# Kernel tuning notes

Measured on AMD Instinct MI355X. Metric: run time of the kernel, lower is better.

The kernel has to match this reference:

```python
import jax, jax.numpy as jnp
import numpy as np

C = 1.0          # Poincare ball curvature
EPS = 1e-7
MAX_TANH_ARG = 1.0 - 1e-5
K = 5            # topk neighbors (hardcoded in the module)


def _norm(x):
    return jnp.clip(jnp.linalg.norm(x, axis=-1, keepdims=True), EPS)


def expmap0(u):
    # exp map at origin: tanh(sqrt(c)||u||) * u / (sqrt(c)||u||)
    sc = jnp.sqrt(C)
    n = _norm(u)
    return jnp.tanh(sc * n) * u / (sc * n)


def logmap0(x):
    # log map at origin: artanh(sqrt(c)||x||) * x / (sqrt(c)||x||)
    sc = jnp.sqrt(C)
    n = _norm(x)
    arg = jnp.clip(sc * n, EPS, MAX_TANH_ARG)
    return jnp.arctanh(arg) * x / (sc * n)


def mobius_add(x, y):
    x2 = jnp.sum(x * x, axis=-1, keepdims=True)
    y2 = jnp.sum(y * y, axis=-1, keepdims=True)
    xy = jnp.sum(x * y, axis=-1, keepdims=True)
    num = (1.0 + 2.0 * C * xy + C * y2) * x + (1.0 - C * x2) * y
    den = 1.0 + 2.0 * C * xy + (C * C) * x2 * y2
    return num / (den + EPS)


def setup_inputs() -> dict:
    key = jax.random.key(0)
    k1, k2, k3, k4 = jax.random.split(key, 4)
    B, SEQ_DIM, HYP_DIM, N = 2048, 768, 128, 100000
    z_seq = jax.random.normal(k1, (B, SEQ_DIM), dtype=jnp.float32)
    # node embeddings must lie inside the unit ball; scale keeps norms ~0.57
    node_emb = 0.05 * jax.random.normal(k2, (N, HYP_DIM), dtype=jnp.float32)
    W = 0.02 * jax.random.normal(k3, (HYP_DIM, SEQ_DIM), dtype=jnp.float32)
    b = jnp.zeros((HYP_DIM,), dtype=jnp.float32)
    return {"z_seq": z_seq, "node_emb": node_emb, "W": W, "b": b}


def reference(z_seq, node_emb, W, b):
    # linear projection (dropout is identity in eval mode)
    z_proj = z_seq @ W.T + b                     # (B, D)
    z_hyp = expmap0(z_proj)                      # (B, D) in Poincare ball
    # no-grad nearest-node lookup in tangent space
    z_tan = logmap0(z_hyp)                       # (B, D)
    n_tan = logmap0(node_emb)                    # (N, D)
    # squared euclidean distances (monotone in cdist -> same topk indices)
    d2 = (jnp.sum(z_tan * z_tan, axis=-1, keepdims=True)
          - 2.0 * (z_tan @ n_tan.T)
          + jnp.sum(n_tan * n_tan, axis=-1)[None, :])  # (B, N)
    _, idx = jax.lax.top_k(-d2, K)               # (B, K) smallest distances
    near = jnp.mean(node_emb[idx], axis=1)       # (B, D) gather-mean
    z_fused = mobius_add(z_hyp, near)
    return (z_fused, z_hyp)
```

## Files before the change

kernel.cpp:

```cpp
#include <hip/hip_runtime.h>
#include <hip/hip_bf16.h>
#include <math.h>

#define EPSF 1e-7f
#define MAXT 0.99999f

typedef __attribute__((ext_vector_type(8))) short short8v;
typedef __attribute__((ext_vector_type(4))) float f32x4;

constexpr int Bb = 2048;
constexpr int Ss = 768;
constexpr int Dd = 128;
constexpr int Nn = 100000;
constexpr int Kk = 5;
constexpr int HALF = Bb * Dd;
constexpr int NT = 128;
constexpr int TILE_BYTES = NT * Dd * 2;
constexpr int SUP_BYTES = 2 * TILE_BYTES;
constexpr float SBIAS = 16.0f;

constexpr int NCH8 = 8;
constexpr int CH8 = Nn / NCH8;
constexpr int TIL8 = 98;
constexpr int NSUP = TIL8 / 2;
constexpr int PAD8 = TIL8 * NT;
constexpr int RQ = 64;

constexpr int NCH16 = 16;
constexpr int CH16 = Nn / NCH16;
constexpr int TIL16 = (CH16 + NT - 1) / NT;
constexpr int RT = 128;

static __device__ __forceinline__ ushort f2bf(float x) {
  __hip_bfloat16 h = __float2bfloat16(x);
  return *reinterpret_cast<ushort*>(&h);
}

static __device__ __forceinline__ float med3f(float a, float b, float c) {
  float r;
  asm("v_med3_f32 %0, %1, %2, %3" : "=v"(r) : "v"(a), "v"(b), "v"(c));
  return r;
}

static __device__ __forceinline__ void ins5f(float* k, float v) {
  const float n0 = fminf(k[0], v);
  const float n1 = med3f(k[0], k[1], v);
  const float n2 = med3f(k[1], k[2], v);
  const float n3 = med3f(k[2], k[3], v);
  const float n4 = med3f(k[3], k[4], v);
  k[0] = n0; k[1] = n1; k[2] = n2; k[3] = n3; k[4] = n4;
}

#define INS5(TV, TI, V, ID) do { \
  const float _v = (V); const int _id = (ID); \
  if (_v < TV[4]) { \
    TV[4] = _v; TI[4] = _id; \
    if (TV[4] < TV[3]) { float _t=TV[3];TV[3]=TV[4];TV[4]=_t;int _u=TI[3];TI[3]=TI[4];TI[4]=_u; } \
    if (TV[3] < TV[2]) { float _t=TV[2];TV[2]=TV[3];TV[3]=_t;int _u=TI[2];TI[2]=TI[3];TI[3]=_u; } \
    if (TV[2] < TV[1]) { float _t=TV[1];TV[1]=TV[2];TV[2]=_t;int _u=TI[1];TI[1]=TI[2];TI[2]=_u; } \
    if (TV[1] < TV[0]) { float _t=TV[0];TV[0]=TV[1];TV[1]=_t;int _u=TI[0];TI[0]=TI[1];TI[1]=_u; } \
  } } while(0)

#define LXLT(V,I,V2,I2) ((V) < (V2) || ((V) == (V2) && (I) < (I2)))
#define INS5L(TV, TI, V, ID) do { \
  const float _v = (V); const int _id = (ID); \
  if (LXLT(_v,_id,TV[4],TI[4])) { \
    TV[4]=_v; TI[4]=_id; \
    if (LXLT(TV[4],TI[4],TV[3],TI[3])) { float _t=TV[3];TV[3]=TV[4];TV[4]=_t;int _u=TI[3];TI[3]=TI[4];TI[4]=_u; } \
    if (LXLT(TV[3],TI[3],TV[2],TI[2])) { float _t=TV[2];TV[2]=TV[3];TV[3]=_t;int _u=TI[2];TI[2]=TI[3];TI[3]=_u; } \
    if (LXLT(TV[2],TI[2],TV[1],TI[1])) { float _t=TV[1];TV[1]=TV[2];TV[2]=_t;int _u=TI[1];TI[1]=TI[2];TI[2]=_u; } \
    if (LXLT(TV[1],TI[1],TV[0],TI[0])) { float _t=TV[0];TV[0]=TV[1];TV[1]=_t;int _u=TI[0];TI[0]=TI[1];TI[1]=_u; } \
  } } while(0)

static __device__ __forceinline__ void proj_body(
    const float* __restrict__ zseq, const float* __restrict__ W,
    const float* __restrict__ bias, float* __restrict__ outH,
    ushort* __restrict__ ztb, int blk,
    float (*zrow)[768], float (*zp)[128], float (*php)[128], float* rno)
{
  const int tid = threadIdx.x;
  const int d = tid & 127, h = tid >> 7;
  const int r0 = blk * 8;

  {
    const float4* src = reinterpret_cast<const float4*>(zseq + (size_t)r0 * Ss);
    float4* dst = reinterpret_cast<float4*>(&zrow[0][0]);
    #pragma unroll
    for (int i = 0; i < 6; ++i) dst[i * 256 + tid] = src[i * 256 + tid];
  }
  __syncthreads();

  float acc[8];
  #pragma unroll
  for (int r = 0; r < 8; ++r) acc[r] = 0.f;
  const float4* w4 = reinterpret_cast<const float4*>(W + (size_t)d * Ss) + h * 96;
  for (int j = 0; j < 96; ++j) {
    const float4 w = w4[j];
    const int kb = h * 384 + j * 4;
    #pragma unroll
    for (int r = 0; r < 8; ++r) {
      const float4 z = *reinterpret_cast<const float4*>(&zrow[r][kb]);
      acc[r] = fmaf(z.x, w.x, acc[r]);
      acc[r] = fmaf(z.y, w.y, acc[r]);
      acc[r] = fmaf(z.z, w.z, acc[r]);
      acc[r] = fmaf(z.w, w.w, acc[r]);
    }
  }
  #pragma unroll
  for (int r = 0; r < 8; ++r) {
    if (h == 0) zp[r][d] = acc[r]; else php[r][d] = acc[r];
  }
  __syncthreads();
  if (tid < 128) {
    const float bv = bias[d];
    #pragma unroll
    for (int r = 0; r < 8; ++r) zp[r][d] = zp[r][d] + php[r][d] + bv;
  }
  __syncthreads();

  const int wv = tid >> 6, ln = tid & 63;
  if (tid < 128) {
    #pragma unroll
    for (int rr = 0; rr < 4; ++rr) {
      const int r = wv * 4 + rr;
      float v = zp[r][ln] * zp[r][ln] + zp[r][ln + 64] * zp[r][ln + 64];
      #pragma unroll
      for (int off = 32; off > 0; off >>= 1) v += __shfl_xor(v, off);
      if (ln == 0) rno[r] = v;
    }
  }
  __syncthreads();
  if (tid < 128) {
    #pragma unroll
    for (int r = 0; r < 8; ++r) {
      const float n = fmaxf(sqrtf(rno[r]), EPSF);
      const float zh = tanhf(n) * zp[r][d] / n;
      outH[(size_t)(r0 + r) * Dd + d] = zh;
      zp[r][d] = zh;
    }
  }
  __syncthreads();
  if (tid < 128) {
    #pragma unroll
    for (int rr = 0; rr < 4; ++rr) {
      const int r = wv * 4 + rr;
      float v = zp[r][ln] * zp[r][ln] + zp[r][ln + 64] * zp[r][ln + 64];
      #pragma unroll
      for (int off = 32; off > 0; off >>= 1) v += __shfl_xor(v, off);
      if (ln == 0) rno[r] = v;
    }
  }
  __syncthreads();
  if (tid < 128) {
    #pragma unroll
    for (int r = 0; r < 8; ++r) {
      const float m = fmaxf(sqrtf(rno[r]), EPSF);
      const float a = atanhf(fminf(m, MAXT));
      ztb[(size_t)(r0 + r) * Dd + d] = f2bf(a * zp[r][d] / m);
    }
  }
}

__global__ __launch_bounds__(256) void k_proj(
    const float* __restrict__ zseq, const float* __restrict__ W,
    const float* __restrict__ bias, float* __restrict__ outH,
    ushort* __restrict__ ztb)
{
  __shared__ __align__(16) float zrow[8][768];
  __shared__ float zp[8][128];
  __shared__ float php[8][128];
  __shared__ float rno[8];
  proj_body(zseq, W, bias, outH, ztb, blockIdx.x, zrow, zp, php, rno);
}

__global__ __launch_bounds__(256) void k_prep(
    const float* __restrict__ zseq, const float* __restrict__ W,
    const float* __restrict__ bias, float* __restrict__ outH,
    ushort* __restrict__ ztb, const float* __restrict__ emb,
    ushort* __restrict__ embsw, float* __restrict__ cpad)
{
  __shared__ __align__(16) float zrow[8][768];
  __shared__ float zp[8][128];
  __shared__ float php[8][128];
  __shared__ float rno[8];

  if (blockIdx.x < Bb / 8) {
    proj_body(zseq, W, bias, outH, ztb, blockIdx.x, zrow, zp, php, rno);
    return;
  }

  const int wv = threadIdx.x >> 6, ln = threadIdx.x & 63;
  const int p = (blockIdx.x - Bb / 8) * 4 + wv;
  const int chunk = p / PAD8;
  const int local = p - chunk * PAD8;
  const bool real = local < CH8;
  const int node = chunk * CH8 + local;
  float2 v = make_float2(0.f, 0.f);
  if (real) v = *reinterpret_cast<const float2*>(emb + (size_t)node * Dd + ln * 2);
  float t = v.x * v.x + v.y * v.y;
  #pragma unroll
  for (int off = 32; off > 0; off >>= 1) t += __shfl_xor(t, off);

  const float E = fmaxf(sqrtf(t), EPSF);
  const float a = atanhf(fminf(E, MAXT));
  const float s = a / E;
  const float m2s = -2.f * s;

  const int tt = local >> 7, nd = local & 127;
  ushort2 w; w.x = f2bf(m2s * v.x); w.y = f2bf(m2s * v.y);
  char* dst = reinterpret_cast<char*>(embsw)
            + ((size_t)((chunk * TIL8 + tt) * NT + nd) << 8)
            + ((ln * 4) ^ ((nd & 7) << 4));
  *reinterpret_cast<ushort2*>(dst) = w;

  if (ln == 0) cpad[p] = real ? (s * s * t + SBIAS) : 3.0e38f;
}

__global__ __launch_bounds__(1024, 4) void k_topk8(
    const ushort* __restrict__ ztb, const ushort* __restrict__ embsw,
    const float* __restrict__ cpad, float* __restrict__ candV,
    int* __restrict__ candI)
{
  __shared__ __align__(16) ushort Bsm[2][2][NT * Dd];
  __shared__ __align__(16) float cb[2][2 * NT];

  const int tid = threadIdx.x;
  const int ln = tid & 63;
  const int wv8 = (tid >> 6) & 7;
  const int qh = tid >> 9;
  const int ln15 = ln & 15;
  const int g = ln >> 4;
  const int chunk = blockIdx.x & 7;
  const int rowBase = (blockIdx.x >> 3) * RQ;
  const int qBase = rowBase + qh * 32;
  const char* embc = reinterpret_cast<const char*>(embsw)
                   + (size_t)chunk * (TIL8 * TILE_BYTES);
  const float* cch = cpad + (size_t)chunk * PAD8;

  short8v zfr[2][4];
  #pragma unroll
  for (int f = 0; f < 2; ++f)
    #pragma unroll
    for (int ks = 0; ks < 4; ++ks)
      zfr[f][ks] = *reinterpret_cast<const short8v*>(
          ztb + (size_t)(qBase + 16 * f + ln15) * Dd + 32 * ks + 8 * g);

  int rdoff[4];
  #pragma unroll
  for (int ks = 0; ks < 4; ++ks)
    rdoff[ks] = (wv8 * 16 + ln15) * 256 + ((ks * 64 + g * 16) ^ ((ln15 & 7) << 4));
  const int coff = wv8 * 64 + g * 16;
  const unsigned lanebase = (unsigned)(wv8 * 16 + 4 * g);

  float tv0[5], tv1[5];
  const float KINIT = __uint_as_float(0x7F7FFFFFu);
  #pragma unroll
  for (int q = 0; q < 5; ++q) { tv0[q] = KINIT; tv1[q] = KINIT; }

  const char* srcP = embc + tid * 16;
  const float* cbP = cch + tid;

  auto stage = [&](int buf) {
    char* lb = reinterpret_cast<char*>(&Bsm[buf][0][0]) + tid * 16;
    #pragma unroll
    for (int i = 0; i < 4; ++i) {
      __builtin_amdgcn_global_load_lds(
          (const __attribute__((address_space(1))) unsigned int*)(srcP + i * 16384),
          (__attribute__((address_space(3))) unsigned int*)(lb + i * 16384),
          16, 0, 0);
    }
    if (tid < 2 * NT) {
      __builtin_amdgcn_global_load_lds(
          (const __attribute__((address_space(1))) unsigned int*)cbP,
          (__attribute__((address_space(3))) unsigned int*)(&cb[buf][tid]),
          4, 0, 0);
    }
    srcP += SUP_BYTES;
    cbP += 2 * NT;
  };

  asm volatile("s_waitcnt vmcnt(0)" ::: "memory");
  stage(0);
  stage(1);

  for (int st = 0; st < NSUP; ++st) {
    const int buf = st & 1;
    if (st == NSUP - 1) {
      asm volatile("s_waitcnt vmcnt(0)" ::: "memory");
    } else if (tid < 2 * NT) {
      asm volatile("s_waitcnt vmcnt(5)" ::: "memory");
    } else {
      asm volatile("s_waitcnt vmcnt(4)" ::: "memory");
    }
    __builtin_amdgcn_s_barrier();

    float mm0 = KINIT, mm1 = KINIT;
    #pragma unroll
    for (int u = 0; u < 2; ++u) {
      const char* bbase = reinterpret_cast<const char*>(&Bsm[buf][u][0]);
      short8v ae[4];
      #pragma unroll
      for (int ks = 0; ks < 4; ++ks)
        ae[ks] = *reinterpret_cast<const short8v*>(bbase + rdoff[ks]);
      const f32x4 cinit = *reinterpret_cast<const f32x4*>(
          reinterpret_cast<const char*>(&cb[buf][u * NT]) + coff);

      __builtin_amdgcn_s_setprio(1);
      f32x4 a0 = __builtin_amdgcn_mfma_f32_16x16x32_bf16(ae[0], zfr[0][0], cinit, 0, 0, 0);
      f32x4 a1 = __builtin_amdgcn_mfma_f32_16x16x32_bf16(ae[0], zfr[1][0], cinit, 0, 0, 0);
      #pragma unroll
      for (int ks = 1; ks < 4; ++ks) {
        a0 = __builtin_amdgcn_mfma_f32_16x16x32_bf16(ae[ks], zfr[0][ks], a0, 0, 0, 0);
        a1 = __builtin_amdgcn_mfma_f32_16x16x32_bf16(ae[ks], zfr[1][ks], a1, 0, 0, 0);
      }
      __builtin_amdgcn_s_setprio(0);

      const unsigned ib = (unsigned)((2 * st + u) * NT) + lanebase;
      {
        const float k0 = __uint_as_float((__float_as_uint(a0[0]) & 0xFFFFC000u) | ib);
        const float k1 = __uint_as_float((__float_as_uint(a0[1]) & 0xFFFFC000u) | (ib + 1));
        const float k2 = __uint_as_float((__float_as_uint(a0[2]) & 0xFFFFC000u) | (ib + 2));
        const float k3 = __uint_as_float((__float_as_uint(a0[3]) & 0xFFFFC000u) | (ib + 3));
        mm0 = fminf(mm0, fminf(fminf(k0, k1), fminf(k2, k3)));
      }
      {
        const float k0 = __uint_as_float((__float_as_uint(a1[0]) & 0xFFFFC000u) | ib);
        const float k1 = __uint_as_float((__float_as_uint(a1[1]) & 0xFFFFC000u) | (ib + 1));
        const float k2 = __uint_as_float((__float_as_uint(a1[2]) & 0xFFFFC000u) | (ib + 2));
        const float k3 = __uint_as_float((__float_as_uint(a1[3]) & 0xFFFFC000u) | (ib + 3));
        mm1 = fminf(mm1, fminf(fminf(k0, k1), fminf(k2, k3)));
      }
    }
    ins5f(tv0, mm0);
    ins5f(tv1, mm1);

    __builtin_amdgcn_s_barrier();
    asm volatile("" ::: "memory");
    if (st + 2 < NSUP) stage(buf);
  }

  #pragma unroll
  for (int m = 16; m <= 32; m <<= 1) {
    float ov[5];
    #pragma unroll
    for (int q = 0; q < 5; ++q) ov[q] = __shfl_xor(tv0[q], m);
    #pragma unroll
    for (int q = 0; q < 5; ++q) ins5f(tv0, ov[q]);
    #pragma unroll
    for (int q = 0; q < 5; ++q) ov[q] = __shfl_xor(tv1[q], m);
    #pragma unroll
    for (int q = 0; q < 5; ++q) ins5f(tv1, ov[q]);
  }
  __syncthreads();
  float* mgk = reinterpret_cast<float*>(&Bsm[0][0][0]);
  if (ln < 16) {
    #pragma unroll
    for (int q = 0; q < 5; ++q) {
      mgk[((qh * 32 + 0 + ln) * 8 + wv8) * Kk + q] = tv0[q];
      mgk[((qh * 32 + 16 + ln) * 8 + wv8) * Kk + q] = tv1[q];
    }
  }
  __syncthreads();
  if (tid < RQ) {
    float mv[5];
    #pragma unroll
    for (int q = 0; q < 5; ++q) mv[q] = mgk[(tid * 8 + 0) * Kk + q];
    for (int w = 1; w < 8; ++w)
      #pragma unroll
      for (int q = 0; q < 5; ++q) ins5f(mv, mgk[(tid * 8 + w) * Kk + q]);
    const size_t o = ((size_t)(rowBase + tid) * NCH8 + chunk) * Kk;
    #pragma unroll
    for (int q = 0; q < 5; ++q) {
      const unsigned u = __float_as_uint(mv[q]);
      candV[o + q] = __uint_as_float(u & 0xFFFFC000u);
      candI[o + q] = chunk * CH8 + (int)(u & 0x3FFFu);
    }
  }
}

__global__ __launch_bounds__(256) void k_node(
    const float* __restrict__ emb, float* __restrict__ sArr, float* __restrict__ cArr)
{
  const int wv = threadIdx.x >> 6, ln = threadIdx.x & 63;
  const int node = blockIdx.x * 4 + wv;
  const float2 v = *reinterpret_cast<const float2*>(emb + (size_t)node * Dd + ln * 2);
  float t = v.x * v.x + v.y * v.y;
  #pragma unroll
  for (int off = 32; off > 0; off >>= 1) t += __shfl_xor(t, off);
  if (ln == 0) {
    const float E = fmaxf(sqrtf(t), EPSF);
    const float a = atanhf(fminf(E, MAXT));
    const float s = a / E;
    sArr[node] = s;
    cArr[node] = s * s * t;
  }
}

__global__ __launch_bounds__(512, 2) void k_topk16(
    const ushort* __restrict__ ztb, const float* __restrict__ emb,
    const float* __restrict__ sArr, const float* __restrict__ cArr,
    float* __restrict__ candV, int* __restrict__ candI)
{
  __shared__ __align__(16) ushort Bsm[2][NT * Dd];
  __shared__ __align__(16) float2 sclb[2][NT];
  __shared__ __align__(16) float mgv[RT][2][Kk];
  __shared__ int mgi[RT][2][Kk];

  const int tid = threadIdx.x;
  const int ln = tid & 63;
  const int wv = tid >> 6;
  const int ln15 = ln & 15;
  const int g = ln >> 4;
  const int wr = wv >> 1;
  const int wc = wv & 1;
  const int rowBase = blockIdx.x * RT;
  const int chunkStart = blockIdx.y * CH16;

  short8v afr[2][4];
  #pragma unroll
  for (int f = 0; f < 2; ++f)
    #pragma unroll
    for (int ks = 0; ks < 4; ++ks)
      afr[f][ks] = *reinterpret_cast<const short8v*>(
          ztb + (size_t)(rowBase + 32 * wr + 16 * f + ln15) * Dd + 32 * ks + 8 * g);

  int rdoff[4];
  #pragma unroll
  for (int ks = 0; ks < 4; ++ks)
    rdoff[ks] = (wc * 64 + ln15) * 256 + ((g * 16 + ks * 64) ^ ((ln15 & 7) << 4));

  f32x4 acc[2][4];
  #pragma unroll
  for (int f = 0; f < 2; ++f)
    #pragma unroll
    for (int c = 0; c < 4; ++c) acc[f][c] = (f32x4)0.f;

  float tv[8][5]; int ti[8][5];
  #pragma unroll
  for (int r = 0; r < 8; ++r)
    #pragma unroll
    for (int q = 0; q < 5; ++q) { tv[r][q] = 3.0e38f; ti[r][q] = 0x7fffffff; }

  float4 ld[8];

  auto stageLoad = [&](int t) {
    const int tStart = t * NT;
    const int left = CH16 - tStart;
    #pragma unroll
    for (int i = 0; i < 8; ++i) {
      const int flat = i * 512 + tid;
      const int nd = flat >> 5;
      float4 v = make_float4(0.f, 0.f, 0.f, 0.f);
      if (nd < left)
        v = *reinterpret_cast<const float4*>(
            emb + (size_t)(chunkStart + tStart + nd) * Dd + (flat & 31) * 4);
      ld[i] = v;
    }
  };

  auto stageWrite = [&](int t, int buf) {
    char* base = reinterpret_cast<char*>(&Bsm[buf][0]);
    #pragma unroll
    for (int i = 0; i < 8; ++i) {
      const int flat = i * 512 + tid;
      const int nd = flat >> 5;
      const int kb = (flat & 31) * 8;
      ushort4 w;
      w.x = f2bf(ld[i].x); w.y = f2bf(ld[i].y);
      w.z = f2bf(ld[i].z); w.w = f2bf(ld[i].w);
      *reinterpret_cast<ushort4*>(base + nd * 256 + (kb ^ ((nd & 7) << 4))) = w;
    }
    const int tStart = t * NT;
    const int left = CH16 - tStart;
    if (tid < NT) {
      const bool ok = tid < left;
      sclb[buf][tid] = make_float2(ok ? -2.f * sArr[chunkStart + tStart + tid] : 0.f,
                                   ok ? cArr[chunkStart + tStart + tid] : 3.0e38f);
    }
  };

  stageLoad(0);
  stageWrite(0, 0);
  __syncthreads();

  for (int t = 0; t < TIL16; ++t) {
    const int buf = t & 1;
    const bool have = (t + 1) < TIL16;
    if (have) stageLoad(t + 1);

    const char* bbase = reinterpret_cast<const char*>(&Bsm[buf][0]);
    #pragma unroll
    for (int c = 0; c < 4; ++c) {
      #pragma unroll
      for (int ks = 0; ks < 4; ++ks) {
        const short8v bfr = *reinterpret_cast<const short8v*>(bbase + c * 4096 + rdoff[ks]);
        acc[0][c] = __builtin_amdgcn_mfma_f32_16x16x32_bf16(afr[0][ks], bfr, acc[0][c], 0, 0, 0);
        acc[1][c] = __builtin_amdgcn_mfma_f32_16x16x32_bf16(afr[1][ks], bfr, acc[1][c], 0, 0, 0);
      }
    }

    if (have) stageWrite(t + 1, buf ^ 1);

    #pragma unroll
    for (int c = 0; c < 4; ++c) {
      const int nl = wc * 64 + c * 16 + ln15;
      const float2 sc2 = sclb[buf][nl];
      const int node = chunkStart + t * NT + nl;
      #pragma unroll
      for (int f = 0; f < 2; ++f) {
        #pragma unroll
        for (int i = 0; i < 4; ++i) {
          const float v = fmaf(sc2.x, acc[f][c][i], sc2.y);
          INS5(tv[f * 4 + i], ti[f * 4 + i], v, node);
        }
        acc[f][c] = (f32x4)0.f;
      }
    }
    __syncthreads();
  }

  #pragma unroll
  for (int m = 1; m <= 8; m <<= 1) {
    #pragma unroll
    for (int r = 0; r < 8; ++r) {
      float ov[5]; int oi[5];
      #pragma unroll
      for (int q = 0; q < 5; ++q) {
        ov[q] = __shfl_xor(tv[r][q], m);
        oi[q] = __shfl_xor(ti[r][q], m);
      }
      #pragma unroll
      for (int q = 0; q < 5; ++q) INS5L(tv[r], ti[r], ov[q], oi[q]);
    }
  }
  if (ln15 == 0) {
    #pragma unroll
    for (int f = 0; f < 2; ++f)
      #pragma unroll
      for (int i = 0; i < 4; ++i) {
        const int row = 32 * wr + 16 * f + 4 * g + i;
        #pragma unroll
        for (int q = 0; q < 5; ++q) {
          mgv[row][wc][q] = tv[f * 4 + i][q];
          mgi[row][wc][q] = ti[f * 4 + i][q];
        }
      }
  }
  __syncthreads();
  if (tid < RT) {
    float mv[5]; int mi[5];
    #pragma unroll
    for (int q = 0; q < 5; ++q) { mv[q] = mgv[tid][0][q]; mi[q] = mgi[tid][0][q]; }
    #pragma unroll
    for (int q = 0; q < 5; ++q) INS5L(mv, mi, mgv[tid][1][q], mgi[tid][1][q]);
    const size_t o = ((size_t)(rowBase + tid) * NCH16 + blockIdx.y) * Kk;
    #pragma unroll
    for (int q = 0; q < 5; ++q) { candV[o + q] = mv[q]; candI[o + q] = mi[q]; }
  }
}

__global__ __launch_bounds__(256) void k_fuse(
    const float* __restrict__ emb, const float* __restrict__ candV,
    const int* __restrict__ candI, const float* __restrict__ zhyp,
    float* __restrict__ out, int ncand)
{
  const int wv = threadIdx.x >> 6, ln = threadIdx.x & 63;
  const int row = blockIdx.x * 4 + wv;

  float mv[5]; int mi[5];
  #pragma unroll
  for (int q = 0; q < 5; ++q) { mv[q] = 3.0e38f; mi[q] = 0x7fffffff; }
  const size_t base = (size_t)row * ncand;
  for (int j = ln; j < ncand; j += 64) INS5L(mv, mi, candV[base + j], candI[base + j]);
  #pragma unroll
  for (int m = 1; m <= 32; m <<= 1) {
    float ov[5]; int oi[5];
    #pragma unroll
    for (int q = 0; q < 5; ++q) { ov[q] = __shfl_xor(mv[q], m); oi[q] = __shfl_xor(mi[q], m); }
    #pragma unroll
    for (int q = 0; q < 5; ++q) INS5L(mv, mi, ov[q], oi[q]);
  }
  float y0 = 0.f, y1 = 0.f;
  #pragma unroll
  for (int q = 0; q < Kk; ++q) {
    const float* e = emb + (size_t)mi[q] * Dd;
    y0 += e[ln]; y1 += e[ln + 64];
  }
  y0 *= 0.2f; y1 *= 0.2f;
  const float x0 = zhyp[(size_t)row * Dd + ln];
  const float x1 = zhyp[(size_t)row * Dd + ln + 64];
  float x2 = x0 * x0 + x1 * x1;
  float y2 = y0 * y0 + y1 * y1;
  float xy = x0 * y0 + x1 * y1;
  #pragma unroll
  for (int off = 32; off > 0; off >>= 1) {
    x2 += __shfl_xor(x2, off);
    y2 += __shfl_xor(y2, off);
    xy += __shfl_xor(xy, off);
  }
  const float ca = 1.f + 2.f * xy + y2;
  const float cb2 = 1.f - x2;
  const float den = 1.f / (1.f + 2.f * xy + x2 * y2 + EPSF);
  out[(size_t)row * Dd + ln] = (ca * x0 + cb2 * y0) * den;
  out[(size_t)row * Dd + ln + 64] = (ca * x1 + cb2 * y1) * den;
}

extern "C" void kernel_launch(void* const* d_in, const int* in_sizes, int n_in,
                              void* d_out, int out_size, void* d_ws, size_t ws_size,
                              hipStream_t stream)
{
  (void)in_sizes; (void)n_in; (void)out_size;
  const float* zseq = (const float*)d_in[0];
  const float* emb  = (const float*)d_in[1];
  const float* W    = (const float*)d_in[2];
  const float* bias = (const float*)d_in[3];
  float* out = (float*)d_out;

  const size_t ztbBytes   = (size_t)Bb * Dd * 2;
  const size_t embswBytes = (size_t)NCH8 * TIL8 * TILE_BYTES;
  const size_t cpadBytes  = (size_t)NCH8 * PAD8 * 4;
  const size_t candVBytes = (size_t)Bb * NCH8 * Kk * 4;
  const size_t needFast = ztbBytes + embswBytes + cpadBytes + 2 * candVBytes;

  if (ws_size >= needFast) {
    char* ws = (char*)d_ws;
    ushort* ztb   = (ushort*)ws;
    ushort* embsw = (ushort*)(ws + ztbBytes);
    float*  cpad  = (float*)(ws + ztbBytes + embswBytes);
    float*  candV = (float*)(ws + ztbBytes + embswBytes + cpadBytes);
    int*    candI = (int*)(ws + ztbBytes + embswBytes + cpadBytes + candVBytes);

    hipLaunchKernelGGL(k_prep, dim3(Bb / 8 + NCH8 * PAD8 / 4), dim3(256), 0,
                       stream, zseq, W, bias, out + HALF, ztb, emb, embsw, cpad);
    hipLaunchKernelGGL(k_topk8, dim3(256), dim3(1024), 0, stream,
                       ztb, embsw, cpad, candV, candI);
    hipLaunchKernelGGL(k_fuse, dim3(Bb / 4), dim3(256), 0, stream,
                       emb, candV, candI, out + HALF, out, NCH8 * Kk);
  } else {
    char* ws = (char*)d_ws;
    ushort* ztb  = (ushort*)ws;
    float* sArr  = (float*)(ws + ztbBytes);
    float* cArr  = sArr + Nn;
    float* candV = cArr + Nn;
    int*   candI = (int*)(candV + (size_t)Bb * NCH16 * Kk);

    hipLaunchKernelGGL(k_proj, dim3(Bb / 8), dim3(256), 0, stream,
                       zseq, W, bias, out + HALF, ztb);
    hipLaunchKernelGGL(k_node, dim3(Nn / 4), dim3(256), 0, stream, emb, sArr, cArr);
    hipLaunchKernelGGL(k_topk16, dim3(Bb / RT, NCH16), dim3(512), 0, stream,
                       ztb, emb, sArr, cArr, candV, candI);
    hipLaunchKernelGGL(k_fuse, dim3(Bb / 4), dim3(256), 0, stream,
                       emb, candV, candI, out + HALF, out, NCH16 * Kk);
  }
}
```

Baseline: 131.9 us.

## Load bias vectors into registers, unroll topk pipeline, widen node prep loads

The topk kernel now loads the per-node bias values straight into registers with inline global_load_dwordx4 instead of staging them through LDS. This removes the cb shared buffer and the tid-dependent vmcnt waits. The super-tile loop is manually unrolled into macros with ping-pong register buffers and a uniform vmcnt(6) wait, plus sched_barriers. The prep kernel handles two nodes per wave using float4 loads and ushort4 stores, which halves the grid. The risks are register pressure under launch_bounds(1024,4) and fragile hand-counted waitcnts.

```diff
diff --git a/kernel.cpp b/kernel.cpp
--- a/kernel.cpp
+++ b/kernel.cpp
@@ -190,16 +190,17 @@
   }
 
   const int wv = threadIdx.x >> 6, ln = threadIdx.x & 63;
-  const int p = (blockIdx.x - Bb / 8) * 4 + wv;
+  const int half = ln >> 5, l5 = ln & 31;
+  const int p = (blockIdx.x - Bb / 8) * 8 + wv * 2 + half;
   const int chunk = p / PAD8;
   const int local = p - chunk * PAD8;
   const bool real = local < CH8;
   const int node = chunk * CH8 + local;
-  float2 v = make_float2(0.f, 0.f);
-  if (real) v = *reinterpret_cast<const float2*>(emb + (size_t)node * Dd + ln * 2);
-  float t = v.x * v.x + v.y * v.y;
-  #pragma unroll
-  for (int off = 32; off > 0; off >>= 1) t += __shfl_xor(t, off);
+  float4 v = make_float4(0.f, 0.f, 0.f, 0.f);
+  if (real) v = *reinterpret_cast<const float4*>(emb + (size_t)node * Dd + l5 * 4);
+  float t = v.x * v.x + v.y * v.y + v.z * v.z + v.w * v.w;
+  #pragma unroll
+  for (int off = 16; off > 0; off >>= 1) t += __shfl_xor(t, off);
 
   const float E = fmaxf(sqrtf(t), EPSF);
   const float a = atanhf(fminf(E, MAXT));
@@ -207,13 +208,15 @@
   const float m2s = -2.f * s;
 
   const int tt = local >> 7, nd = local & 127;
-  ushort2 w; w.x = f2bf(m2s * v.x); w.y = f2bf(m2s * v.y);
+  ushort4 w;
+  w.x = f2bf(m2s * v.x); w.y = f2bf(m2s * v.y);
+  w.z = f2bf(m2s * v.z); w.w = f2bf(m2s * v.w);
   char* dst = reinterpret_cast<char*>(embsw)
             + ((size_t)((chunk * TIL8 + tt) * NT + nd) << 8)
-            + ((ln * 4) ^ ((nd & 7) << 4));
-  *reinterpret_cast<ushort2*>(dst) = w;
-
-  if (ln == 0) cpad[p] = real ? (s * s * t + SBIAS) : 3.0e38f;
+            + ((l5 * 8) ^ ((nd & 7) << 4));
+  *reinterpret_cast<ushort4*>(dst) = w;
+
+  if (l5 == 0) cpad[p] = real ? (s * s * t + SBIAS) : 3.0e38f;
 }
 
 __global__ __launch_bounds__(1024, 4) void k_topk8(
@@ -222,7 +225,6 @@
     int* __restrict__ candI)
 {
   __shared__ __align__(16) ushort Bsm[2][2][NT * Dd];
-  __shared__ __align__(16) float cb[2][2 * NT];
 
   const int tid = threadIdx.x;
   const int ln = tid & 63;
@@ -249,7 +251,6 @@
   #pragma unroll
   for (int ks = 0; ks < 4; ++ks)
     rdoff[ks] = (wv8 * 16 + ln15) * 256 + ((ks * 64 + g * 16) ^ ((ln15 & 7) << 4));
-  const int coff = wv8 * 64 + g * 16;
   const unsigned lanebase = (unsigned)(wv8 * 16 + 4 * g);
 
   float tv0[5], tv1[5];
@@ -258,86 +259,92 @@
   for (int q = 0; q < 5; ++q) { tv0[q] = KINIT; tv1[q] = KINIT; }
 
   const char* srcP = embc + tid * 16;
-  const float* cbP = cch + tid;
-
-  auto stage = [&](int buf) {
-    char* lb = reinterpret_cast<char*>(&Bsm[buf][0][0]) + tid * 16;
-    #pragma unroll
-    for (int i = 0; i < 4; ++i) {
-      __builtin_amdgcn_global_load_lds(
-          (const __attribute__((address_space(1))) unsigned int*)(srcP + i * 16384),
-          (__attribute__((address_space(3))) unsigned int*)(lb + i * 16384),
-          16, 0, 0);
-    }
-    if (tid < 2 * NT) {
-      __builtin_amdgcn_global_load_lds(
-          (const __attribute__((address_space(1))) unsigned int*)cbP,
-          (__attribute__((address_space(3))) unsigned int*)(&cb[buf][tid]),
-          4, 0, 0);
-    }
-    srcP += SUP_BYTES;
-    cbP += 2 * NT;
-  };
+  unsigned long long cvP =
+      (unsigned long long)(cch + wv8 * 16 + 4 * g);
+
+  f32x4 cvA0, cvA1, cvB0, cvB1;
+
+#define STAGE(BB, CV0, CV1) do { \
+    char* lb = reinterpret_cast<char*>(&Bsm[BB][0][0]) + tid * 16; \
+    __builtin_amdgcn_global_load_lds( \
+        (const __attribute__((address_space(1))) unsigned int*)(srcP), \
+        (__attribute__((address_space(3))) unsigned int*)(lb), 16, 0, 0); \
+    __builtin_amdgcn_global_load_lds( \
+        (const __attribute__((address_space(1))) unsigned int*)(srcP + 16384), \
+        (__attribute__((address_space(3))) unsigned int*)(lb + 16384), 16, 0, 0); \
+    __builtin_amdgcn_global_load_lds( \
+        (const __attribute__((address_space(1))) unsigned int*)(srcP + 32768), \
+        (__attribute__((address_space(3))) unsigned int*)(lb + 32768), 16, 0, 0); \
+    __builtin_amdgcn_global_load_lds( \
+        (const __attribute__((address_space(1))) unsigned int*)(srcP + 49152), \
+        (__attribute__((address_space(3))) unsigned int*)(lb + 49152), 16, 0, 0); \
+    asm volatile("global_load_dwordx4 %0, %2, off\n\t" \
+                 "global_load_dwordx4 %1, %3, off" \
+        : "=&v"(CV0), "=&v"(CV1) \
+        : "v"(cvP), "v"(cvP + (unsigned long long)(NT * 4))); \
+    srcP += SUP_BYTES; \
+    cvP += (unsigned long long)(2 * NT * 4); } while (0)
+
+#define TILEBODY(BB, UU, CV, IBV, MM0, MM1) do { \
+    const char* bbase = reinterpret_cast<const char*>(&Bsm[BB][UU][0]); \
+    const short8v ae0 = *reinterpret_cast<const short8v*>(bbase + rdoff[0]); \
+    const short8v ae1 = *reinterpret_cast<const short8v*>(bbase + rdoff[1]); \
+    const short8v ae2 = *reinterpret_cast<const short8v*>(bbase + rdoff[2]); \
+    const short8v ae3 = *reinterpret_cast<const short8v*>(bbase + rdoff[3]); \
+    __builtin_amdgcn_s_setprio(1); \
+    f32x4 a0 = __builtin_amdgcn_mfma_f32_16x16x32_bf16(ae0, zfr[0][0], CV, 0, 0, 0); \
+    f32x4 a1 = __builtin_amdgcn_mfma_f32_16x16x32_bf16(ae0, zfr[1][0], CV, 0, 0, 0); \
+    a0 = __builtin_amdgcn_mfma_f32_16x16x32_bf16(ae1, zfr[0][1], a0, 0, 0, 0); \
+    a1 = __builtin_amdgcn_mfma_f32_16x16x32_bf16(ae1, zfr[1][1], a1, 0, 0, 0); \
+    a0 = __builtin_amdgcn_mfma_f32_16x16x32_bf16(ae2, zfr[0][2], a0, 0, 0, 0); \
+    a1 = __builtin_amdgcn_mfma_f32_16x16x32_bf16(ae2, zfr[1][2], a1, 0, 0, 0); \
+    a0 = __builtin_amdgcn_mfma_f32_16x16x32_bf16(ae3, zfr[0][3], a0, 0, 0, 0); \
+    a1 = __builtin_amdgcn_mfma_f32_16x16x32_bf16(ae3, zfr[1][3], a1, 0, 0, 0); \
+    __builtin_amdgcn_s_setprio(0); \
+    const unsigned ibv = (IBV); \
+    { const float k0 = __uint_as_float((__float_as_uint(a0[0]) & 0xFFFFC000u) | ibv); \
+      const float k1 = __uint_as_float((__float_as_uint(a0[1]) & 0xFFFFC000u) | (ibv + 1)); \
+      const float k2 = __uint_as_float((__float_as_uint(a0[2]) & 0xFFFFC000u) | (ibv + 2)); \
+      const float k3 = __uint_as_float((__float_as_uint(a0[3]) & 0xFFFFC000u) | (ibv + 3)); \
+      MM0 = fminf(MM0, fminf(fminf(k0, k1), fminf(k2, k3))); } \
+    { const float k0 = __uint_as_float((__float_as_uint(a1[0]) & 0xFFFFC000u) | ibv); \
+      const float k1 = __uint_as_float((__float_as_uint(a1[1]) & 0xFFFFC000u) | (ibv + 1)); \
+      const float k2 = __uint_as_float((__float_as_uint(a1[2]) & 0xFFFFC000u) | (ibv + 2)); \
+      const float k3 = __uint_as_float((__float_as_uint(a1[3]) & 0xFFFFC000u) | (ibv + 3)); \
+      MM1 = fminf(MM1, fminf(fminf(k0, k1), fminf(k2, k3))); } \
+  } while (0)
+
+#define PROCSUP(BB, CV0, CV1, ST, WN) do { \
+    asm volatile("s_waitcnt vmcnt(" #WN ")" ::: "memory"); \
+    __builtin_amdgcn_sched_barrier(0); \
+    __builtin_amdgcn_s_barrier(); \
+    float mm0 = KINIT, mm1 = KINIT; \
+    TILEBODY(BB, 0, CV0, (unsigned)((2 * (ST)) * NT) + lanebase, mm0, mm1); \
+    TILEBODY(BB, 1, CV1, (unsigned)((2 * (ST) + 1) * NT) + lanebase, mm0, mm1); \
+    ins5f(tv0, mm0); \
+    ins5f(tv1, mm1); \
+    __builtin_amdgcn_s_barrier(); \
+    asm volatile("" ::: "memory"); \
+  } while (0)
 
   asm volatile("s_waitcnt vmcnt(0)" ::: "memory");
-  stage(0);
-  stage(1);
-
-  for (int st = 0; st < NSUP; ++st) {
-    const int buf = st & 1;
-    if (st == NSUP - 1) {
-      asm volatile("s_waitcnt vmcnt(0)" ::: "memory");
-    } else if (tid < 2 * NT) {
-      asm volatile("s_waitcnt vmcnt(5)" ::: "memory");
-    } else {
-      asm volatile("s_waitcnt vmcnt(4)" ::: "memory");
-    }
-    __builtin_amdgcn_s_barrier();
-
-    float mm0 = KINIT, mm1 = KINIT;
-    #pragma unroll
-    for (int u = 0; u < 2; ++u) {
-      const char* bbase = reinterpret_cast<const char*>(&Bsm[buf][u][0]);
-      short8v ae[4];
-      #pragma unroll
-      for (int ks = 0; ks < 4; ++ks)
-        ae[ks] = *reinterpret_cast<const short8v*>(bbase + rdoff[ks]);
-      const f32x4 cinit = *reinterpret_cast<const f32x4*>(
-          reinterpret_cast<const char*>(&cb[buf][u * NT]) + coff);
-
-      __builtin_amdgcn_s_setprio(1);
-      f32x4 a0 = __builtin_amdgcn_mfma_f32_16x16x32_bf16(ae[0], zfr[0][0], cinit, 0, 0, 0);
-      f32x4 a1 = __builtin_amdgcn_mfma_f32_16x16x32_bf16(ae[0], zfr[1][0], cinit, 0, 0, 0);
-      #pragma unroll
-      for (int ks = 1; ks < 4; ++ks) {
-        a0 = __builtin_amdgcn_mfma_f32_16x16x32_bf16(ae[ks], zfr[0][ks], a0, 0, 0, 0);
-        a1 = __builtin_amdgcn_mfma_f32_16x16x32_bf16(ae[ks], zfr[1][ks], a1, 0, 0, 0);
-      }
-      __builtin_amdgcn_s_setprio(0);
-
-      const unsigned ib = (unsigned)((2 * st + u) * NT) + lanebase;
-      {
-        const float k0 = __uint_as_float((__float_as_uint(a0[0]) & 0xFFFFC000u) | ib);
-        const float k1 = __uint_as_float((__float_as_uint(a0[1]) & 0xFFFFC000u) | (ib + 1));
-        const float k2 = __uint_as_float((__float_as_uint(a0[2]) & 0xFFFFC000u) | (ib + 2));
-        const float k3 = __uint_as_float((__float_as_uint(a0[3]) & 0xFFFFC000u) | (ib + 3));
-        mm0 = fminf(mm0, fminf(fminf(k0, k1), fminf(k2, k3)));
-      }
-      {
-        const float k0 = __uint_as_float((__float_as_uint(a1[0]) & 0xFFFFC000u) | ib);
-        const float k1 = __uint_as_float((__float_as_uint(a1[1]) & 0xFFFFC000u) | (ib + 1));
-        const float k2 = __uint_as_float((__float_as_uint(a1[2]) & 0xFFFFC000u) | (ib + 2));
-        const float k3 = __uint_as_float((__float_as_uint(a1[3]) & 0xFFFFC000u) | (ib + 3));
-        mm1 = fminf(mm1, fminf(fminf(k0, k1), fminf(k2, k3)));
-      }
-    }
-    ins5f(tv0, mm0);
-    ins5f(tv1, mm1);
-
-    __builtin_amdgcn_s_barrier();
-    asm volatile("" ::: "memory");
-    if (st + 2 < NSUP) stage(buf);
-  }
+  STAGE(0, cvA0, cvA1);
+  STAGE(1, cvB0, cvB1);
+
+  for (int ss = 0; ss < 23; ++ss) {
+    PROCSUP(0, cvA0, cvA1, 2 * ss, 6);
+    STAGE(0, cvA0, cvA1);
+    PROCSUP(1, cvB0, cvB1, 2 * ss + 1, 6);
+    STAGE(1, cvB0, cvB1);
+  }
+  PROCSUP(0, cvA0, cvA1, 46, 6);
+  STAGE(0, cvA0, cvA1);
+  PROCSUP(1, cvB0, cvB1, 47, 6);
+  PROCSUP(0, cvA0, cvA1, 48, 0);
+
+#undef STAGE
+#undef TILEBODY
+#undef PROCSUP
 
   #pragma unroll
   for (int m = 16; m <= 32; m <<= 1) {
@@ -630,7 +637,7 @@
     float*  candV = (float*)(ws + ztbBytes + embswBytes + cpadBytes);
     int*    candI = (int*)(ws + ztbBytes + embswBytes + cpadBytes + candVBytes);
 
-    hipLaunchKernelGGL(k_prep, dim3(Bb / 8 + NCH8 * PAD8 / 4), dim3(256), 0,
+    hipLaunchKernelGGL(k_prep, dim3(Bb / 8 + NCH8 * PAD8 / 8), dim3(256), 0,
                        stream, zseq, W, bias, out + HALF, ztb, emb, embsw, cpad);
     hipLaunchKernelGGL(k_topk8, dim3(256), dim3(1024), 0, stream,
                        ztb, embsw, cpad, candV, candI);
```

After: 116.5 us (median of 2 runs). -11.7%, faster.
